# Kernel optimization log

Measured on AMD Instinct MI355X. Metric: run time of the kernel, lower is better.

## Reference

```python
import jax, jax.numpy as jnp
import numpy as np

M, K, N = 8192, 4096, 4096  # tokens, in_features, out_features
QMAX = 127.0


def setup_inputs() -> dict:
    key = jax.random.key(0)
    kx, kw, ks, kb = jax.random.split(key, 4)
    x = jax.random.normal(kx, (M, K), dtype=jnp.float32)
    # Build w_q / s_w the same way from_float would: per-output-channel symmetric quant
    w = jax.random.normal(kw, (N, K), dtype=jnp.float32) * 0.02
    s_w = (jnp.max(jnp.abs(w), axis=1, keepdims=True) / QMAX).astype(jnp.float32)  # [N,1]
    w_q = jnp.clip(jnp.round(w / s_w), -QMAX, QMAX).astype(jnp.int8)  # [N,K] int8
    bias = jax.random.normal(kb, (N,), dtype=jnp.float32) * 0.01
    return {"x": x, "w_q": w_q, "s_w": s_w, "bias": bias}


def reference(x, w_q, s_w, bias):
    # mode == 'W8A8_dynamic': per-tensor symmetric activation quant (zp = 0)
    s_x = jnp.max(jnp.abs(x)) / QMAX                       # scalar scale
    x_q = jnp.clip(jnp.round(x / s_x), -QMAX, QMAX)        # int8 values held in fp32
    # fake-dequant matmul: (x_q @ w_q^T) * (s_x * s_w^T) + bias
    y_int = x_q @ w_q.astype(jnp.float32).T                # [M, N]
    y = y_int * (s_x * s_w.astype(jnp.float32).T)          # broadcast [1,N]
    y = y + bias
    return y.astype(x.dtype)
```

## Files before the change

### kernel.cpp

```cpp
#include <hip/hip_runtime.h>
#include <stdint.h>

#define QMAXF 127.0f

constexpr int Mdim = 8192;
constexpr int Kdim = 4096;
constexpr int Ndim = 4096;
constexpr int PREP_BLOCKS = 2048;

using i32x4 = __attribute__((ext_vector_type(4))) int;

__device__ __forceinline__ void async_copy16(const void* g, void* l) {
    __builtin_amdgcn_global_load_lds(
        (const __attribute__((address_space(1))) void*)g,
        (__attribute__((address_space(3))) void*)l,
        16, 0, 0);
}

__global__ void prep_kernel(const float* __restrict__ x,
                            const int* __restrict__ w32,
                            float* __restrict__ blockmax,
                            int8_t* __restrict__ w8) {
    float m = 0.f;
    const float4* x4 = (const float4*)x;
    const int n4x = Mdim * Kdim / 4;
    for (int i = blockIdx.x * blockDim.x + threadIdx.x; i < n4x;
         i += gridDim.x * blockDim.x) {
        float4 v = x4[i];
        m = fmaxf(fmaxf(fabsf(v.x), fabsf(v.y)),
                  fmaxf(m, fmaxf(fabsf(v.z), fabsf(v.w))));
    }
#pragma unroll
    for (int off = 32; off > 0; off >>= 1)
        m = fmaxf(m, __shfl_down(m, off, 64));
    __shared__ float red[4];
    if ((threadIdx.x & 63) == 0) red[threadIdx.x >> 6] = m;
    __syncthreads();
    if (threadIdx.x == 0)
        blockmax[blockIdx.x] =
            fmaxf(fmaxf(red[0], red[1]), fmaxf(red[2], red[3]));

    const int4* in4 = (const int4*)w32;
    char4* out4 = (char4*)w8;
    const int n4w = Ndim * Kdim / 4;
    for (int i = blockIdx.x * blockDim.x + threadIdx.x; i < n4w;
         i += gridDim.x * blockDim.x) {
        int4 v = in4[i];
        char4 c;
        c.x = (signed char)v.x;
        c.y = (signed char)v.y;
        c.z = (signed char)v.z;
        c.w = (signed char)v.w;
        out4[i] = c;
    }
}

__global__ void finalize_kernel(const float* __restrict__ blockmax,
                                float* __restrict__ sx) {
    float m = 0.f;
    for (int i = threadIdx.x; i < PREP_BLOCKS; i += 256)
        m = fmaxf(m, blockmax[i]);
#pragma unroll
    for (int off = 32; off > 0; off >>= 1)
        m = fmaxf(m, __shfl_down(m, off, 64));
    __shared__ float red[4];
    if ((threadIdx.x & 63) == 0) red[threadIdx.x >> 6] = m;
    __syncthreads();
    if (threadIdx.x == 0)
        *sx = fmaxf(fmaxf(red[0], red[1]), fmaxf(red[2], red[3])) / QMAXF;
}

__global__ void quant_x_kernel(const float* __restrict__ x,
                               const float* __restrict__ sxp,
                               int8_t* __restrict__ xq, int n4) {
    const float s = *sxp;
    const float4* x4 = (const float4*)x;
    char4* q4 = (char4*)xq;
    for (int i = blockIdx.x * blockDim.x + threadIdx.x; i < n4;
         i += gridDim.x * blockDim.x) {
        float4 v = x4[i];
        char4 q;
        q.x = (signed char)(int)fminf(QMAXF, fmaxf(-QMAXF, rintf(v.x / s)));
        q.y = (signed char)(int)fminf(QMAXF, fmaxf(-QMAXF, rintf(v.y / s)));
        q.z = (signed char)(int)fminf(QMAXF, fmaxf(-QMAXF, rintf(v.z / s)));
        q.w = (signed char)(int)fminf(QMAXF, fmaxf(-QMAXF, rintf(v.w / s)));
        q4[i] = q;
    }
}

#define BM 128
#define BN 128
#define BK 128

__global__ __launch_bounds__(256) void gemm_i8_kernel(
    const int8_t* __restrict__ Xq, const int8_t* __restrict__ Wq,
    const float* __restrict__ sxp, const float* __restrict__ s_w,
    const float* __restrict__ bias, float* __restrict__ Y) {
    __shared__ int8_t As[BM * BK];
    __shared__ int8_t Bs[BN * BK];

    const int t = threadIdx.x;
    const int w = t >> 6;
    const int l = t & 63;
    const int lane15 = l & 15;
    const int lquad = l >> 4;
    const int swz = lane15 & 7;
    const int wm = (w >> 1) * 64;
    const int wn = (w & 1) * 64;

    const int bm = blockIdx.y * BM;
    const int bn = blockIdx.x * BN;

    const int8_t* aptr[4];
    const int8_t* bptr[4];
#pragma unroll
    for (int s = 0; s < 4; s++) {
        const int cl = t + 256 * s;
        const int r = cl >> 3;
        const int c = ((cl & 7) ^ (r & 7)) * 16;
        aptr[s] = Xq + (size_t)(bm + r) * Kdim + c;
        bptr[s] = Wq + (size_t)(bn + r) * Kdim + c;
    }
    int8_t* alds[4];
    int8_t* blds[4];
#pragma unroll
    for (int s = 0; s < 4; s++) {
        alds[s] = As + s * 4096 + w * 1024;
        blds[s] = Bs + s * 4096 + w * 1024;
    }

    i32x4 acc[4][4] = {};

    for (int kt = 0; kt < Kdim; kt += BK) {
#pragma unroll
        for (int s = 0; s < 4; s++) async_copy16(aptr[s] + kt, alds[s]);
#pragma unroll
        for (int s = 0; s < 4; s++) async_copy16(bptr[s] + kt, blds[s]);
        __syncthreads();

#pragma unroll
        for (int kk = 0; kk < 2; kk++) {
            i32x4 a[4], b[4];
#pragma unroll
            for (int i = 0; i < 4; i++)
                a[i] = *(const i32x4*)(As + (wm + i * 16 + lane15) * BK +
                                       (((kk << 2) | lquad) ^ swz) * 16);
#pragma unroll
            for (int j = 0; j < 4; j++)
                b[j] = *(const i32x4*)(Bs + (wn + j * 16 + lane15) * BK +
                                       (((kk << 2) | lquad) ^ swz) * 16);
#pragma unroll
            for (int i = 0; i < 4; i++)
#pragma unroll
                for (int j = 0; j < 4; j++)
                    acc[i][j] = __builtin_amdgcn_mfma_i32_16x16x64_i8(
                        a[i], b[j], acc[i][j], 0, 0, 0);
        }
        __syncthreads();
    }

    const float sx = *sxp;
#pragma unroll
    for (int j = 0; j < 4; j++) {
        const int col = bn + wn + j * 16 + lane15;
        const float sc = sx * s_w[col];
        const float bs = bias[col];
#pragma unroll
        for (int i = 0; i < 4; i++) {
            const int row = bm + wm + i * 16 + lquad * 4;
            float* yp = Y + (size_t)row * Ndim + col;
#pragma unroll
            for (int r = 0; r < 4; r++)
                yp[(size_t)r * Ndim] = (float)acc[i][j][r] * sc + bs;
        }
    }
}

extern "C" void kernel_launch(void* const* d_in, const int* in_sizes, int n_in,
                              void* d_out, int out_size, void* d_ws,
                              size_t ws_size, hipStream_t stream) {
    const float* x = (const float*)d_in[0];
    const int* w_q = (const int*)d_in[1];
    const float* s_w = (const float*)d_in[2];
    const float* bias = (const float*)d_in[3];
    float* y = (float*)d_out;

    float* sx = (float*)d_ws;
    float* blockmax = (float*)((char*)d_ws + 256);
    int8_t* xq = (int8_t*)d_ws + 16384;
    int8_t* wq8 = (int8_t*)d_ws + 16384 + (size_t)Mdim * Kdim;

    prep_kernel<<<PREP_BLOCKS, 256, 0, stream>>>(x, w_q, blockmax, wq8);
    finalize_kernel<<<1, 256, 0, stream>>>(blockmax, sx);
    quant_x_kernel<<<PREP_BLOCKS, 256, 0, stream>>>(x, sx, xq,
                                                    Mdim * Kdim / 4);

    dim3 grid(Ndim / BN, Mdim / BM);
    gemm_i8_kernel<<<grid, 256, 0, stream>>>(xq, wq8, sx, s_w, bias, y);
}
```

Measured before the change: 431.9 us.

## Fuse abs-max, finalize and quantize into one cooperative kernel with grid sync

Merges the three preprocessing kernels (block abs-max plus weight narrowing, global max finalize, activation quantization) into a single cooperative launch that uses a grid-wide barrier between the reduction and quantization phases. Each block redundantly reduces the 1024 block maxima to get the scale. This removes two kernel launches and their gaps, and may give some L2 reuse of x between the max pass and the quantize pass. The cost is halving the prep grid to 1024 blocks to fit co-residency, plus the grid-sync overhead.

Result: slower. 540.1 us (+25.0%).

```diff
diff --git a/kernel.cpp b/kernel.cpp
--- a/kernel.cpp
+++ b/kernel.cpp
@@ -1,12 +1,15 @@
 #include <hip/hip_runtime.h>
+#include <hip/hip_cooperative_groups.h>
 #include <stdint.h>
+
+namespace cg = cooperative_groups;
 
 #define QMAXF 127.0f
 
 constexpr int Mdim = 8192;
 constexpr int Kdim = 4096;
 constexpr int Ndim = 4096;
-constexpr int PREP_BLOCKS = 2048;
+constexpr int PREP_BLOCKS = 1024;
 
 using i32x4 = __attribute__((ext_vector_type(4))) int;
 
@@ -17,15 +20,18 @@
         16, 0, 0);
 }
 
-__global__ void prep_kernel(const float* __restrict__ x,
-                            const int* __restrict__ w32,
-                            float* __restrict__ blockmax,
-                            int8_t* __restrict__ w8) {
+__global__ __launch_bounds__(256) void prep_coop_kernel(
+    const float* __restrict__ x, const int* __restrict__ w32,
+    float* __restrict__ blockmax, int8_t* __restrict__ w8,
+    int8_t* __restrict__ xq, float* __restrict__ sxp) {
+    const int n4x = Mdim * Kdim / 4;
+    const int n4w = Ndim * Kdim / 4;
+    const int gstride = PREP_BLOCKS * 256;
+    const int gtid = blockIdx.x * 256 + threadIdx.x;
+
     float m = 0.f;
     const float4* x4 = (const float4*)x;
-    const int n4x = Mdim * Kdim / 4;
-    for (int i = blockIdx.x * blockDim.x + threadIdx.x; i < n4x;
-         i += gridDim.x * blockDim.x) {
+    for (int i = gtid; i < n4x; i += gstride) {
         float4 v = x4[i];
         m = fmaxf(fmaxf(fabsf(v.x), fabsf(v.y)),
                   fmaxf(m, fmaxf(fabsf(v.z), fabsf(v.w))));
@@ -42,9 +48,7 @@
 
     const int4* in4 = (const int4*)w32;
     char4* out4 = (char4*)w8;
-    const int n4w = Ndim * Kdim / 4;
-    for (int i = blockIdx.x * blockDim.x + threadIdx.x; i < n4w;
-         i += gridDim.x * blockDim.x) {
+    for (int i = gtid; i < n4w; i += gstride) {
         int4 v = in4[i];
         char4 c;
         c.x = (signed char)v.x;
@@ -53,31 +57,30 @@
         c.w = (signed char)v.w;
         out4[i] = c;
     }
-}
-
-__global__ void finalize_kernel(const float* __restrict__ blockmax,
-                                float* __restrict__ sx) {
-    float m = 0.f;
+
+    cg::this_grid().sync();
+
+    float gm = 0.f;
     for (int i = threadIdx.x; i < PREP_BLOCKS; i += 256)
-        m = fmaxf(m, blockmax[i]);
+        gm = fmaxf(gm, blockmax[i]);
 #pragma unroll
     for (int off = 32; off > 0; off >>= 1)
-        m = fmaxf(m, __shfl_down(m, off, 64));
-    __shared__ float red[4];
-    if ((threadIdx.x & 63) == 0) red[threadIdx.x >> 6] = m;
+        gm = fmaxf(gm, __shfl_down(gm, off, 64));
+    __shared__ float red2[4];
+    if ((threadIdx.x & 63) == 0) red2[threadIdx.x >> 6] = gm;
     __syncthreads();
-    if (threadIdx.x == 0)
-        *sx = fmaxf(fmaxf(red[0], red[1]), fmaxf(red[2], red[3])) / QMAXF;
-}
-
-__global__ void quant_x_kernel(const float* __restrict__ x,
-                               const float* __restrict__ sxp,
-                               int8_t* __restrict__ xq, int n4) {
-    const float s = *sxp;
-    const float4* x4 = (const float4*)x;
+    __shared__ float s_sh;
+    if (threadIdx.x == 0) {
+        const float s =
+            fmaxf(fmaxf(red2[0], red2[1]), fmaxf(red2[2], red2[3])) / QMAXF;
+        s_sh = s;
+        if (blockIdx.x == 0) *sxp = s;
+    }
+    __syncthreads();
+    const float s = s_sh;
+
     char4* q4 = (char4*)xq;
-    for (int i = blockIdx.x * blockDim.x + threadIdx.x; i < n4;
-         i += gridDim.x * blockDim.x) {
+    for (int i = gtid; i < n4x; i += gstride) {
         float4 v = x4[i];
         char4 q;
         q.x = (signed char)(int)fminf(QMAXF, fmaxf(-QMAXF, rintf(v.x / s)));
@@ -190,10 +193,10 @@
     int8_t* xq = (int8_t*)d_ws + 16384;
     int8_t* wq8 = (int8_t*)d_ws + 16384 + (size_t)Mdim * Kdim;
 
-    prep_kernel<<<PREP_BLOCKS, 256, 0, stream>>>(x, w_q, blockmax, wq8);
-    finalize_kernel<<<1, 256, 0, stream>>>(blockmax, sx);
-    quant_x_kernel<<<PREP_BLOCKS, 256, 0, stream>>>(x, sx, xq,
-                                                    Mdim * Kdim / 4);
+    void* args[] = {(void*)&x,   (void*)&w_q, (void*)&blockmax,
+                    (void*)&wq8, (void*)&xq,  (void*)&sx};
+    hipLaunchCooperativeKernel((const void*)prep_coop_kernel,
+                               dim3(PREP_BLOCKS), dim3(256), args, 0, stream);
 
     dim3 grid(Ndim / BN, Mdim / BM);
     gemm_i8_kernel<<<grid, 256, 0, stream>>>(xq, wq8, sx, s_w, bias, y);
```
